# Performance work log

Hardware: AMD Instinct MI355X
Metric: run time of the kernel (lower is better)

## Reference

```python
import jax, jax.numpy as jnp
import numpy as np

B, T, IN_DIM = 128, 512, 32
H = 256            # h_dim; bidirectional -> embedding_dim D = 2*H = 512
N_EMB = 1024
BETA = 0.25


def setup_inputs() -> dict:
    key = jax.random.key(0)
    ks = jax.random.split(key, 12)
    traj = jax.random.normal(ks[0], (B, T, IN_DIM), dtype=jnp.float32)
    # variable-length padding mask: ones up to length, zeros after
    lengths = jax.random.randint(ks[1], (B,), 1, T + 1)
    mask = (jnp.arange(T)[None, :] < lengths[:, None]).astype(jnp.int32)
    s_x = 1.0 / np.sqrt(H)
    def u(k, shape):
        return jax.random.uniform(k, shape, jnp.float32, -s_x, s_x)
    # PyTorch GRU param layout: W_ih [3H, in], W_hh [3H, H], biases [3H]
    Wx_f, Wh_f = u(ks[2], (3 * H, IN_DIM)), u(ks[3], (3 * H, H))
    bx_f, bh_f = u(ks[4], (3 * H,)), u(ks[5], (3 * H,))
    Wx_b, Wh_b = u(ks[6], (3 * H, IN_DIM)), u(ks[7], (3 * H, H))
    bx_b, bh_b = u(ks[8], (3 * H,)), u(ks[9], (3 * H,))
    # codebook: nn.Embedding(n_embeddings, D) with uniform(-1/n, 1/n) init
    codebook = jax.random.uniform(ks[10], (N_EMB, 2 * H), jnp.float32,
                                  -1.0 / N_EMB, 1.0 / N_EMB)
    return {"traj": traj, "mask": mask,
            "Wx_f": Wx_f, "Wh_f": Wh_f, "bx_f": bx_f, "bh_f": bh_f,
            "Wx_b": Wx_b, "Wh_b": Wh_b, "bx_b": bx_b, "bh_b": bh_b,
            "codebook": codebook}


def _gru_dir(x, Wx, Wh, bx, bh):
    """Single-direction GRU over time (PyTorch gate math). x: [B,T,in] -> [B,T,H]."""
    b, t, _ = x.shape
    h_dim = Wh.shape[1]
    xg = jnp.einsum('bti,gi->btg', x, Wx) + bx  # precompute input gates [B,T,3H]
    def step(h, xg_t):
        hg = h @ Wh.T + bh
        xr, xz, xn = jnp.split(xg_t, 3, axis=-1)
        hr, hz, hn = jnp.split(hg, 3, axis=-1)
        r = jax.nn.sigmoid(xr + hr)
        z = jax.nn.sigmoid(xz + hz)
        n = jnp.tanh(xn + r * hn)
        h_new = (1.0 - z) * n + z * h
        return h_new, h_new
    h0 = jnp.zeros((b, h_dim), x.dtype)
    _, hs = jax.lax.scan(step, h0, jnp.swapaxes(xg, 0, 1))  # [T,B,H]
    return jnp.swapaxes(hs, 0, 1)


def _encode(traj, Wx_f, Wh_f, bx_f, bh_f, Wx_b, Wh_b, bx_b, bh_b):
    out_f = _gru_dir(traj, Wx_f, Wh_f, bx_f, bh_f)
    out_b = jnp.flip(_gru_dir(jnp.flip(traj, axis=1), Wx_b, Wh_b, bx_b, bh_b), axis=1)
    return jnp.concatenate([out_f, out_b], axis=-1)  # [B,T,2H]


def _vq(z_e, codebook, beta):
    # d(z, e) = |z|^2 + |e|^2 - 2 z.e  -> argmin over codebook
    d = (jnp.sum(z_e ** 2, axis=1, keepdims=True)
         + jnp.sum(codebook ** 2, axis=1)[None, :]
         - 2.0 * z_e @ codebook.T)                      # [B, N_EMB]
    idx = jnp.argmin(d, axis=1)                         # [B]
    z_q = codebook[idx]                                 # gather [B, D]
    loss = (jnp.mean((jax.lax.stop_gradient(z_q) - z_e) ** 2)
            + beta * jnp.mean((z_q - jax.lax.stop_gradient(z_e)) ** 2))
    z_q_st = z_e + jax.lax.stop_gradient(z_q - z_e)     # straight-through
    counts = jnp.zeros((codebook.shape[0],), z_e.dtype).at[idx].add(1.0)
    p = counts / z_e.shape[0]
    perplexity = jnp.exp(-jnp.sum(p * jnp.log(p + 1e-10)))
    return loss, z_q_st, perplexity, idx


def reference(traj, mask, Wx_f, Wh_f, bx_f, bh_f, Wx_b, Wh_b, bx_b, bh_b, codebook):
    z_e = _encode(traj, Wx_f, Wh_f, bx_f, bh_f, Wx_b, Wh_b, bx_b, bh_b)  # [B,T,2H]
    t = mask.shape[1]
    # last index where mask == 1:  T-1 - argmax(flip(mask))
    last_real_index = t - 1 - jnp.argmax(jnp.flip(mask, axis=1), axis=1)
    z_e_last = z_e[jnp.arange(z_e.shape[0]), last_real_index]            # [B,2H]
    loss, z_q, perplexity, _ = _vq(z_e_last, codebook, BETA)
    return z_q, loss, perplexity
```

## Files before the change

### kernel.cpp

```cpp
#include <hip/hip_runtime.h>
#include <math.h>

constexpr int B  = 128;
constexpr int T  = 512;
constexpr int IN = 32;
constexpr int H  = 256;
constexpr int D  = 2 * H;
constexpr int NC = 1024;

constexpr int NG   = 64;
constexpr int GW   = 4;
constexpr int SEQ  = 4;
constexpr int NTHR = 768;


__global__ void k_zero(int* __restrict__ counts, double* __restrict__ lsum) {
    const int i = blockIdx.x * 256 + threadIdx.x;
    if (i < NC) counts[i] = 0;
    if (i == 0) *lsum = 0.0;
}

__global__ void k_lengths(const int* __restrict__ mask, int* __restrict__ last) {
    const int b = blockIdx.x;
    const int t = threadIdx.x;
    int s = 0;
    #pragma unroll
    for (int m = 0; m < T / 64; ++m) s += mask[b * T + m * 64 + t];
    #pragma unroll
    for (int off = 32; off > 0; off >>= 1) s += __shfl_down(s, off, 64);
    if (t == 0) last[b] = s - 1;
}

__global__ void k_plan(const int* __restrict__ last, int* __restrict__ plan,
                       int* __restrict__ slen, int* __restrict__ glen) {
    __shared__ int ll[B];
    const int t = threadIdx.x;
    ll[t] = last[t];
    __syncthreads();
    const int lf = ll[t] + 1;
    const int lb = T - ll[t];
    int rf = 0, rb = 0;
    for (int j = 0; j < B; ++j) {
        const int ljf = ll[j] + 1, ljb = T - ll[j];
        rf += (ljf > lf) || (ljf == lf && j < t);
        rb += (ljb > lb) || (ljb == lb && j < t);
    }
    plan[rf] = t;       slen[rf] = lf;
    plan[128 + rb] = t; slen[128 + rb] = lb;
    if ((rf & 3) == 0) glen[rf >> 2] = lf;
    if ((rb & 3) == 0) glen[32 + (rb >> 2)] = lb;
}

__global__ void k_transpose(float* __restrict__ dst, const float* __restrict__ src,
                            int rows, int cols) {
    const int idx = blockIdx.x * 256 + threadIdx.x;
    const int r = idx % rows;
    const int c = idx / rows;
    dst[idx] = src[r * cols + c];
}

__global__ void k_cbn2(const float* __restrict__ cb, double* __restrict__ cbn2) {
    const int c = blockIdx.x * 256 + threadIdx.x;
    double s = 0.0;
    for (int k = 0; k < D; ++k) {
        const double e = (double)cb[c * D + k];
        s += e * e;
    }
    cbn2[c] = s;
}


__device__ __forceinline__ float sigmoidf_(float x) {
    return 1.0f / (1.0f + expf(-x));
}

__global__ __launch_bounds__(NTHR, 3) void k_gru(
    const float* __restrict__ traj,
    const float* __restrict__ Whf, const float* __restrict__ Whb,
    const float* __restrict__ Wxf, const float* __restrict__ Wxb,
    const float* __restrict__ bxf, const float* __restrict__ bhf,
    const float* __restrict__ bxb, const float* __restrict__ bhb,
    const int* __restrict__ plan, const int* __restrict__ slen,
    const int* __restrict__ glen,
    unsigned long long* __restrict__ hgt,
    float* __restrict__ ze)
{
    const int g   = blockIdx.x & 63;
    const int w   = blockIdx.x >> 6;
    const int dir = (g >= 32) ? 1 : 0;

    const float* __restrict__ Wh = dir ? Whb : Whf;
    const float* __restrict__ Wx = dir ? Wxb : Wxf;
    const float* __restrict__ bx = dir ? bxb : bxf;
    const float* __restrict__ bh = dir ? bhb : bhf;

    const int tid = threadIdx.x;
    const int kq  = tid / 96;
    const int rp  = tid - kq * 96;
    const int lr0 = 2 * rp;
    const int gi  = lr0 >> 6;
    const int Rg0 = gi * H + w * 64 + (lr0 & 63);

    __shared__ float4 h4[SEQ][64];
    __shared__ float  P [8][SEQ][194];
    __shared__ float  Px[8][SEQ][194];
    __shared__ float4 xb4[2][SEQ][8];
    __shared__ int    bbS[SEQ], lsS[SEQ];

    if (tid < SEQ) { bbS[tid] = plan[g * 4 + tid]; lsS[tid] = slen[g * 4 + tid]; }
    {
        float2* hp = (float2*)h4;
        if (tid < 512) hp[tid] = make_float2(0.0f, 0.0f);
    }
    const int L = glen[g];

    float4 wh[16];
    {
        const float4* p0 = (const float4*)(Wh + (size_t)Rg0 * 256 + kq * 32);
        const float4* p1 = (const float4*)(Wh + (size_t)(Rg0 + 1) * 256 + kq * 32);
        #pragma unroll
        for (int i = 0; i < 8; ++i) { wh[i] = p0[i]; wh[8 + i] = p1[i]; }
    }
    const float4 wx0 = *(const float4*)(Wx + Rg0 * 32 + kq * 4);
    const float4 wx1 = *(const float4*)(Wx + (Rg0 + 1) * 32 + kq * 4);

    float bxr = 0, bxz = 0, bxn = 0, bhr = 0, bhz = 0, bhn = 0;
    if (tid < 256) {
        const int j2 = tid & 63;
        bxr = bx[w * 64 + j2]; bxz = bx[H + w * 64 + j2]; bxn = bx[2 * H + w * 64 + j2];
        bhr = bh[w * 64 + j2]; bhz = bh[H + w * 64 + j2]; bhn = bh[2 * H + w * 64 + j2];
    }
    __syncthreads();
    if (tid < 128) {
        const int s = tid >> 5, i = tid & 31;
        const int t0 = dir ? (T - 1) : 0;
        ((float*)xb4)[128 + s * 32 + i] = traj[(bbS[s] * T + t0) * IN + i];
    }
    __syncthreads();

    const int u = tid - 256;

    for (int step = 1; step <= L; ++step) {
        const int buf = step & 1;
        unsigned long long* __restrict__ slab =
            hgt + (buf * NG + g) * (GW * SEQ * 64);

        float4 a0 = {0,0,0,0}, a1 = {0,0,0,0}, a2 = {0,0,0,0}, a3 = {0,0,0,0};
        float4 c0 = {0,0,0,0}, c1 = {0,0,0,0}, c2 = {0,0,0,0}, c3 = {0,0,0,0};
        #pragma unroll
        for (int i = 0; i < 8; ++i) {
            const float4 w0 = wh[i];
            const float4 w1 = wh[8 + i];
            float4 hv;
            hv = h4[0][kq * 8 + i];
            a0.x = fmaf(w0.x, hv.x, a0.x); a0.y = fmaf(w0.y, hv.y, a0.y);
            a0.z = fmaf(w0.z, hv.z, a0.z); a0.w = fmaf(w0.w, hv.w, a0.w);
            c0.x = fmaf(w1.x, hv.x, c0.x); c0.y = fmaf(w1.y, hv.y, c0.y);
            c0.z = fmaf(w1.z, hv.z, c0.z); c0.w = fmaf(w1.w, hv.w, c0.w);
            hv = h4[1][kq * 8 + i];
            a1.x = fmaf(w0.x, hv.x, a1.x); a1.y = fmaf(w0.y, hv.y, a1.y);
            a1.z = fmaf(w0.z, hv.z, a1.z); a1.w = fmaf(w0.w, hv.w, a1.w);
            c1.x = fmaf(w1.x, hv.x, c1.x); c1.y = fmaf(w1.y, hv.y, c1.y);
            c1.z = fmaf(w1.z, hv.z, c1.z); c1.w = fmaf(w1.w, hv.w, c1.w);
            hv = h4[2][kq * 8 + i];
            a2.x = fmaf(w0.x, hv.x, a2.x); a2.y = fmaf(w0.y, hv.y, a2.y);
            a2.z = fmaf(w0.z, hv.z, a2.z); a2.w = fmaf(w0.w, hv.w, a2.w);
            c2.x = fmaf(w1.x, hv.x, c2.x); c2.y = fmaf(w1.y, hv.y, c2.y);
            c2.z = fmaf(w1.z, hv.z, c2.z); c2.w = fmaf(w1.w, hv.w, c2.w);
            hv = h4[3][kq * 8 + i];
            a3.x = fmaf(w0.x, hv.x, a3.x); a3.y = fmaf(w0.y, hv.y, a3.y);
            a3.z = fmaf(w0.z, hv.z, a3.z); a3.w = fmaf(w0.w, hv.w, a3.w);
            c3.x = fmaf(w1.x, hv.x, c3.x); c3.y = fmaf(w1.y, hv.y, c3.y);
            c3.z = fmaf(w1.z, hv.z, c3.z); c3.w = fmaf(w1.w, hv.w, c3.w);
        }
        {
            float4 xv;
            float2 pv;
            xv = xb4[buf][0][kq];
            pv.x = a0.x + a0.y + a0.z + a0.w;
            pv.y = c0.x + c0.y + c0.z + c0.w;
            *(float2*)&P[kq][0][lr0] = pv;
            pv.x = wx0.x * xv.x + wx0.y * xv.y + wx0.z * xv.z + wx0.w * xv.w;
            pv.y = wx1.x * xv.x + wx1.y * xv.y + wx1.z * xv.z + wx1.w * xv.w;
            *(float2*)&Px[kq][0][lr0] = pv;
            xv = xb4[buf][1][kq];
            pv.x = a1.x + a1.y + a1.z + a1.w;
            pv.y = c1.x + c1.y + c1.z + c1.w;
            *(float2*)&P[kq][1][lr0] = pv;
            pv.x = wx0.x * xv.x + wx0.y * xv.y + wx0.z * xv.z + wx0.w * xv.w;
            pv.y = wx1.x * xv.x + wx1.y * xv.y + wx1.z * xv.z + wx1.w * xv.w;
            *(float2*)&Px[kq][1][lr0] = pv;
            xv = xb4[buf][2][kq];
            pv.x = a2.x + a2.y + a2.z + a2.w;
            pv.y = c2.x + c2.y + c2.z + c2.w;
            *(float2*)&P[kq][2][lr0] = pv;
            pv.x = wx0.x * xv.x + wx0.y * xv.y + wx0.z * xv.z + wx0.w * xv.w;
            pv.y = wx1.x * xv.x + wx1.y * xv.y + wx1.z * xv.z + wx1.w * xv.w;
            *(float2*)&Px[kq][2][lr0] = pv;
            xv = xb4[buf][3][kq];
            pv.x = a3.x + a3.y + a3.z + a3.w;
            pv.y = c3.x + c3.y + c3.z + c3.w;
            *(float2*)&P[kq][3][lr0] = pv;
            pv.x = wx0.x * xv.x + wx0.y * xv.y + wx0.z * xv.z + wx0.w * xv.w;
            pv.y = wx1.x * xv.x + wx1.y * xv.y + wx1.z * xv.z + wx1.w * xv.w;
            *(float2*)&Px[kq][3][lr0] = pv;
        }
        __syncthreads();

        if (tid < 256) {
            const int j2 = tid & 63, s = tid >> 6;
            float hr = 0.f, hz = 0.f, hn_ = 0.f, xr = 0.f, xz = 0.f, xn = 0.f;
            #pragma unroll
            for (int kk = 0; kk < 8; ++kk) {
                hr  += P [kk][s][j2];
                hz  += P [kk][s][64 + j2];
                hn_ += P [kk][s][128 + j2];
                xr  += Px[kk][s][j2];
                xz  += Px[kk][s][64 + j2];
                xn  += Px[kk][s][128 + j2];
            }
            const float r = sigmoidf_(xr + bxr + hr + bhr);
            const float z = sigmoidf_(xz + bxz + hz + bhz);
            const float n = tanhf(xn + bxn + r * (hn_ + bhn));
            const int jg = w * 64 + j2;
            const float hp = ((const float*)h4)[s * 256 + jg];
            const float hnew = (1.0f - z) * n + z * hp;
            ((float*)h4)[s * 256 + jg] = hnew;
            union { float f; unsigned ui; } cv; cv.f = hnew;
            const unsigned long long pk =
                ((unsigned long long)(unsigned)step << 32) | cv.ui;
            __hip_atomic_store(&slab[w * 256 + s * 64 + j2], pk,
                               __ATOMIC_RELAXED, __HIP_MEMORY_SCOPE_AGENT);
            if (step == lsS[s]) ze[bbS[s] * D + dir * H + jg] = hnew;
        } else {
            float xval = 0.0f;
            int xs = 0, xi = 0;
            const bool do_x = (u < 128) && (step < L);
            if (do_x) {
                xs = u >> 5; xi = u & 31;
                const int tn = dir ? (T - 1 - step) : step;
                xval = traj[(bbS[xs] * T + tn) * IN + xi];
            }
            const int p0 = u >> 8;
            const int r2 = u & 255;
            const int s0 = r2 >> 6, j0 = r2 & 63;
            const int pw0 = p0 + (p0 >= w ? 1 : 0);
            unsigned long long* ad0 = &slab[pw0 * 256 + s0 * 64 + j0];
            if (u < 256) {
                const int pw1 = 2 + (2 >= w ? 1 : 0);
                unsigned long long* ad1 = &slab[pw1 * 256 + s0 * 64 + j0];
                unsigned long long v0 = 0, v1 = 0;
                bool d0 = false, d1 = false;
                do {
                    if (!d0) { v0 = __hip_atomic_load(ad0, __ATOMIC_RELAXED,
                                   __HIP_MEMORY_SCOPE_AGENT); d0 = ((int)(v0 >> 32) >= step); }
                    if (!d1) { v1 = __hip_atomic_load(ad1, __ATOMIC_RELAXED,
                                   __HIP_MEMORY_SCOPE_AGENT); d1 = ((int)(v1 >> 32) >= step); }
                } while (!(d0 && d1));
                union { unsigned ui; float f; } e0, e1;
                e0.ui = (unsigned)v0; e1.ui = (unsigned)v1;
                ((float*)h4)[s0 * 256 + pw0 * 64 + j0] = e0.f;
                ((float*)h4)[s0 * 256 + pw1 * 64 + j0] = e1.f;
            } else {
                unsigned long long v0;
                do {
                    v0 = __hip_atomic_load(ad0, __ATOMIC_RELAXED,
                                           __HIP_MEMORY_SCOPE_AGENT);
                } while ((int)(v0 >> 32) < step);
                union { unsigned ui; float f; } e0; e0.ui = (unsigned)v0;
                ((float*)h4)[s0 * 256 + pw0 * 64 + j0] = e0.f;
            }
            if (do_x)
                ((float*)xb4)[(buf ^ 1) * 128 + xs * 32 + xi] = xval;
        }
        __syncthreads();
    }
}


__global__ __launch_bounds__(256) void k_vq(
    const float* __restrict__ ze, const float* __restrict__ cbT,
    const float* __restrict__ cb, const double* __restrict__ cbn2,
    int* __restrict__ counts, double* __restrict__ lsum,
    float* __restrict__ out)
{
    __shared__ float lz[D];
    __shared__ double ds[256];
    __shared__ int cs[256];

    const int b = blockIdx.x;
    const int t = threadIdx.x;

    lz[t]       = ze[b * D + t];
    lz[t + 256] = ze[b * D + 256 + t];
    __syncthreads();

    double best = 1e300;
    int bc = 0;
    for (int m = 0; m < NC / 256; ++m) {
        const int c = m * 256 + t;
        double s2 = 0.0;
        #pragma unroll 4
        for (int k = 0; k < D; ++k)
            s2 += (double)lz[k] * (double)cbT[k * NC + c];
        const double dist = cbn2[c] - 2.0 * s2;
        if (dist < best) { best = dist; bc = c; }
    }
    ds[t] = best; cs[t] = bc;
    __syncthreads();
    for (int s = 128; s > 0; s >>= 1) {
        if (t < s) {
            if (ds[t + s] < ds[t] || (ds[t + s] == ds[t] && cs[t + s] < cs[t])) {
                ds[t] = ds[t + s]; cs[t] = cs[t + s];
            }
        }
        __syncthreads();
    }
    const int idx = cs[0];
    __syncthreads();

    if (t == 0) atomicAdd(&counts[idx], 1);

    double loc = 0.0;
    for (int jj = t; jj < D; jj += 256) {
        const float zev = lz[jj];
        const float zqv = cb[idx * D + jj];
        out[b * D + jj] = zev + (zqv - zev);
        const double df = (double)zqv - (double)zev;
        loc += df * df;
    }
    ds[t] = loc;
    __syncthreads();
    for (int s = 128; s > 0; s >>= 1) {
        if (t < s) ds[t] += ds[t + s];
        __syncthreads();
    }
    if (t == 0) atomicAdd(lsum, ds[0]);
}

__global__ void k_final(const int* __restrict__ counts,
                        const double* __restrict__ lsum,
                        float* __restrict__ out)
{
    __shared__ double ds[256];
    const int t = threadIdx.x;
    double s = 0.0;
    for (int c = t; c < NC; c += 256) {
        const double p = (double)counts[c] / (double)B;
        s += p * log(p + 1e-10);
    }
    ds[t] = s;
    __syncthreads();
    for (int r = 128; r > 0; r >>= 1) {
        if (t < r) ds[t] += ds[t + r];
        __syncthreads();
    }
    if (t == 0) {
        out[B * D]     = (float)(lsum[0] * 1.25 / (double)(B * D));
        out[B * D + 1] = (float)exp(-ds[0]);
    }
}


extern "C" void kernel_launch(void* const* d_in, const int* in_sizes, int n_in,
                              void* d_out, int out_size, void* d_ws, size_t ws_size,
                              hipStream_t stream) {
    const float* traj = (const float*)d_in[0];
    const int*   mask = (const int*)d_in[1];
    const float* Wxf  = (const float*)d_in[2];
    const float* Whf  = (const float*)d_in[3];
    const float* bxf  = (const float*)d_in[4];
    const float* bhf  = (const float*)d_in[5];
    const float* Wxb  = (const float*)d_in[6];
    const float* Whb  = (const float*)d_in[7];
    const float* bxb  = (const float*)d_in[8];
    const float* bhb  = (const float*)d_in[9];
    const float* cb   = (const float*)d_in[10];
    float* out = (float*)d_out;

    float* ws    = (float*)d_ws;
    float* cbT   = ws;
    float* zebuf = cbT + 524288;
    unsigned long long* hgt =
        (unsigned long long*)(zebuf + 65536);
    int*   last  = (int*)(hgt + 131072);
    int*   plan  = last + 128;
    int*   slen  = plan + 256;
    int*   glen  = slen + 256;
    int*   cnts  = glen + 64;
    double* cbn2 = (double*)(cnts + 1024 + 4);
    double* lsum = cbn2 + 1024;

    k_zero<<<dim3(4), dim3(256), 0, stream>>>(cnts, lsum);
    k_lengths<<<dim3(B), dim3(64), 0, stream>>>(mask, last);
    k_plan<<<dim3(1), dim3(B), 0, stream>>>(last, plan, slen, glen);

    k_transpose<<<dim3(2048), dim3(256), 0, stream>>>(cbT, cb, NC, D);
    k_cbn2<<<dim3(4), dim3(256), 0, stream>>>(cb, cbn2);

    k_gru<<<dim3(NG * GW), dim3(NTHR), 26880, stream>>>(
        traj, Whf, Whb, Wxf, Wxb, bxf, bhf, bxb, bhb,
        plan, slen, glen, hgt, zebuf);

    k_vq<<<dim3(B), dim3(256), 0, stream>>>(zebuf, cbT, cb, cbn2, cnts, lsum, out);
    k_final<<<dim3(1), dim3(256), 0, stream>>>(cnts, lsum, out);
}
```

Baseline: 1.720 ms.

## Shrink GRU block to 512 threads with three rows per thread

Cuts the GRU block from 768 to 512 threads. Each thread now computes three recurrent weight rows instead of two, keeping 24 float4 weight registers. The next-step input load moves into the gate-update threads. The polling threads each wait on three peer slabs instead of one or two. This reduces thread count and barrier cost per step, but raises register pressure, replaces vectorised float2 shared stores with scalar ones, and makes each polling thread spin on more flags.

After: 1.857 ms. 1.08x slower.

```diff
diff --git a/kernel.cpp b/kernel.cpp
--- a/kernel.cpp
+++ b/kernel.cpp
@@ -11,7 +11,7 @@
 constexpr int NG   = 64;
 constexpr int GW   = 4;
 constexpr int SEQ  = 4;
-constexpr int NTHR = 768;
+constexpr int NTHR = 512;
 
 
 __global__ void k_zero(int* __restrict__ counts, double* __restrict__ lsum) {
@@ -74,7 +74,7 @@
     return 1.0f / (1.0f + expf(-x));
 }
 
-__global__ __launch_bounds__(NTHR, 3) void k_gru(
+__global__ __launch_bounds__(NTHR, 2) void k_gru(
     const float* __restrict__ traj,
     const float* __restrict__ Whf, const float* __restrict__ Whb,
     const float* __restrict__ Wxf, const float* __restrict__ Wxb,
@@ -95,11 +95,12 @@
     const float* __restrict__ bh = dir ? bhb : bhf;
 
     const int tid = threadIdx.x;
-    const int kq  = tid / 96;
-    const int rp  = tid - kq * 96;
-    const int lr0 = 2 * rp;
-    const int gi  = lr0 >> 6;
-    const int Rg0 = gi * H + w * 64 + (lr0 & 63);
+    const int kq  = tid >> 6;
+    const int rt  = tid & 63;
+    const int lrA = 3 * rt, lrB = lrA + 1, lrC = lrA + 2;
+    const int RA = (lrA >> 6) * H + w * 64 + (lrA & 63);
+    const int RB = (lrB >> 6) * H + w * 64 + (lrB & 63);
+    const int RC = (lrC >> 6) * H + w * 64 + (lrC & 63);
 
     __shared__ float4 h4[SEQ][64];
     __shared__ float  P [8][SEQ][194];
@@ -110,19 +111,21 @@
     if (tid < SEQ) { bbS[tid] = plan[g * 4 + tid]; lsS[tid] = slen[g * 4 + tid]; }
     {
         float2* hp = (float2*)h4;
-        if (tid < 512) hp[tid] = make_float2(0.0f, 0.0f);
+        hp[tid] = make_float2(0.0f, 0.0f);
     }
     const int L = glen[g];
 
-    float4 wh[16];
+    float4 wh[24];
     {
-        const float4* p0 = (const float4*)(Wh + (size_t)Rg0 * 256 + kq * 32);
-        const float4* p1 = (const float4*)(Wh + (size_t)(Rg0 + 1) * 256 + kq * 32);
+        const float4* pA = (const float4*)(Wh + (size_t)RA * 256 + kq * 32);
+        const float4* pB = (const float4*)(Wh + (size_t)RB * 256 + kq * 32);
+        const float4* pC = (const float4*)(Wh + (size_t)RC * 256 + kq * 32);
         #pragma unroll
-        for (int i = 0; i < 8; ++i) { wh[i] = p0[i]; wh[8 + i] = p1[i]; }
-    }
-    const float4 wx0 = *(const float4*)(Wx + Rg0 * 32 + kq * 4);
-    const float4 wx1 = *(const float4*)(Wx + (Rg0 + 1) * 32 + kq * 4);
+        for (int i = 0; i < 8; ++i) { wh[i] = pA[i]; wh[8 + i] = pB[i]; wh[16 + i] = pC[i]; }
+    }
+    const float4 wx0 = *(const float4*)(Wx + RA * 32 + kq * 4);
+    const float4 wx1 = *(const float4*)(Wx + RB * 32 + kq * 4);
+    const float4 wx2 = *(const float4*)(Wx + RC * 32 + kq * 4);
 
     float bxr = 0, bxz = 0, bxn = 0, bhr = 0, bhz = 0, bhn = 0;
     if (tid < 256) {
@@ -147,63 +150,72 @@
 
         float4 a0 = {0,0,0,0}, a1 = {0,0,0,0}, a2 = {0,0,0,0}, a3 = {0,0,0,0};
         float4 c0 = {0,0,0,0}, c1 = {0,0,0,0}, c2 = {0,0,0,0}, c3 = {0,0,0,0};
+        float4 e0 = {0,0,0,0}, e1 = {0,0,0,0}, e2 = {0,0,0,0}, e3 = {0,0,0,0};
         #pragma unroll
         for (int i = 0; i < 8; ++i) {
             const float4 w0 = wh[i];
             const float4 w1 = wh[8 + i];
+            const float4 w2 = wh[16 + i];
             float4 hv;
             hv = h4[0][kq * 8 + i];
             a0.x = fmaf(w0.x, hv.x, a0.x); a0.y = fmaf(w0.y, hv.y, a0.y);
             a0.z = fmaf(w0.z, hv.z, a0.z); a0.w = fmaf(w0.w, hv.w, a0.w);
             c0.x = fmaf(w1.x, hv.x, c0.x); c0.y = fmaf(w1.y, hv.y, c0.y);
             c0.z = fmaf(w1.z, hv.z, c0.z); c0.w = fmaf(w1.w, hv.w, c0.w);
+            e0.x = fmaf(w2.x, hv.x, e0.x); e0.y = fmaf(w2.y, hv.y, e0.y);
+            e0.z = fmaf(w2.z, hv.z, e0.z); e0.w = fmaf(w2.w, hv.w, e0.w);
             hv = h4[1][kq * 8 + i];
             a1.x = fmaf(w0.x, hv.x, a1.x); a1.y = fmaf(w0.y, hv.y, a1.y);
             a1.z = fmaf(w0.z, hv.z, a1.z); a1.w = fmaf(w0.w, hv.w, a1.w);
             c1.x = fmaf(w1.x, hv.x, c1.x); c1.y = fmaf(w1.y, hv.y, c1.y);
             c1.z = fmaf(w1.z, hv.z, c1.z); c1.w = fmaf(w1.w, hv.w, c1.w);
+            e1.x = fmaf(w2.x, hv.x, e1.x); e1.y = fmaf(w2.y, hv.y, e1.y);
+            e1.z = fmaf(w2.z, hv.z, e1.z); e1.w = fmaf(w2.w, hv.w, e1.w);
             hv = h4[2][kq * 8 + i];
             a2.x = fmaf(w0.x, hv.x, a2.x); a2.y = fmaf(w0.y, hv.y, a2.y);
             a2.z = fmaf(w0.z, hv.z, a2.z); a2.w = fmaf(w0.w, hv.w, a2.w);
             c2.x = fmaf(w1.x, hv.x, c2.x); c2.y = fmaf(w1.y, hv.y, c2.y);
             c2.z = fmaf(w1.z, hv.z, c2.z); c2.w = fmaf(w1.w, hv.w, c2.w);
+            e2.x = fmaf(w2.x, hv.x, e2.x); e2.y = fmaf(w2.y, hv.y, e2.y);
+            e2.z = fmaf(w2.z, hv.z, e2.z); e2.w = fmaf(w2.w, hv.w, e2.w);
             hv = h4[3][kq * 8 + i];
             a3.x = fmaf(w0.x, hv.x, a3.x); a3.y = fmaf(w0.y, hv.y, a3.y);
             a3.z = fmaf(w0.z, hv.z, a3.z); a3.w = fmaf(w0.w, hv.w, a3.w);
             c3.x = fmaf(w1.x, hv.x, c3.x); c3.y = fmaf(w1.y, hv.y, c3.y);
             c3.z = fmaf(w1.z, hv.z, c3.z); c3.w = fmaf(w1.w, hv.w, c3.w);
+            e3.x = fmaf(w2.x, hv.x, e3.x); e3.y = fmaf(w2.y, hv.y, e3.y);
+            e3.z = fmaf(w2.z, hv.z, e3.z); e3.w = fmaf(w2.w, hv.w, e3.w);
         }
         {
             float4 xv;
-            float2 pv;
             xv = xb4[buf][0][kq];
-            pv.x = a0.x + a0.y + a0.z + a0.w;
-            pv.y = c0.x + c0.y + c0.z + c0.w;
-            *(float2*)&P[kq][0][lr0] = pv;
-            pv.x = wx0.x * xv.x + wx0.y * xv.y + wx0.z * xv.z + wx0.w * xv.w;
-            pv.y = wx1.x * xv.x + wx1.y * xv.y + wx1.z * xv.z + wx1.w * xv.w;
-            *(float2*)&Px[kq][0][lr0] = pv;
+            P[kq][0][lrA] = a0.x + a0.y + a0.z + a0.w;
+            P[kq][0][lrB] = c0.x + c0.y + c0.z + c0.w;
+            P[kq][0][lrC] = e0.x + e0.y + e0.z + e0.w;
+            Px[kq][0][lrA] = wx0.x * xv.x + wx0.y * xv.y + wx0.z * xv.z + wx0.w * xv.w;
+            Px[kq][0][lrB] = wx1.x * xv.x + wx1.y * xv.y + wx1.z * xv.z + wx1.w * xv.w;
+            Px[kq][0][lrC] = wx2.x * xv.x + wx2.y * xv.y + wx2.z * xv.z + wx2.w * xv.w;
             xv = xb4[buf][1][kq];
-            pv.x = a1.x + a1.y + a1.z + a1.w;
-            pv.y = c1.x + c1.y + c1.z + c1.w;
-            *(float2*)&P[kq][1][lr0] = pv;
-            pv.x = wx0.x * xv.x + wx0.y * xv.y + wx0.z * xv.z + wx0.w * xv.w;
-            pv.y = wx1.x * xv.x + wx1.y * xv.y + wx1.z * xv.z + wx1.w * xv.w;
-            *(float2*)&Px[kq][1][lr0] = pv;
+            P[kq][1][lrA] = a1.x + a1.y + a1.z + a1.w;
+            P[kq][1][lrB] = c1.x + c1.y + c1.z + c1.w;
+            P[kq][1][lrC] = e1.x + e1.y + e1.z + e1.w;
+            Px[kq][1][lrA] = wx0.x * xv.x + wx0.y * xv.y + wx0.z * xv.z + wx0.w * xv.w;
+            Px[kq][1][lrB] = wx1.x * xv.x + wx1.y * xv.y + wx1.z * xv.z + wx1.w * xv.w;
+            Px[kq][1][lrC] = wx2.x * xv.x + wx2.y * xv.y + wx2.z * xv.z + wx2.w * xv.w;
             xv = xb4[buf][2][kq];
-            pv.x = a2.x + a2.y + a2.z + a2.w;
-            pv.y = c2.x + c2.y + c2.z + c2.w;
-            *(float2*)&P[kq][2][lr0] = pv;
-            pv.x = wx0.x * xv.x + wx0.y * xv.y + wx0.z * xv.z + wx0.w * xv.w;
-            pv.y = wx1.x * xv.x + wx1.y * xv.y + wx1.z * xv.z + wx1.w * xv.w;
-            *(float2*)&Px[kq][2][lr0] = pv;
+            P[kq][2][lrA] = a2.x + a2.y + a2.z + a2.w;
+            P[kq][2][lrB] = c2.x + c2.y + c2.z + c2.w;
+            P[kq][2][lrC] = e2.x + e2.y + e2.z + e2.w;
+            Px[kq][2][lrA] = wx0.x * xv.x + wx0.y * xv.y + wx0.z * xv.z + wx0.w * xv.w;
+            Px[kq][2][lrB] = wx1.x * xv.x + wx1.y * xv.y + wx1.z * xv.z + wx1.w * xv.w;
+            Px[kq][2][lrC] = wx2.x * xv.x + wx2.y * xv.y + wx2.z * xv.z + wx2.w * xv.w;
             xv = xb4[buf][3][kq];
-            pv.x = a3.x + a3.y + a3.z + a3.w;
-            pv.y = c3.x + c3.y + c3.z + c3.w;
-            *(float2*)&P[kq][3][lr0] = pv;
-            pv.x = wx0.x * xv.x + wx0.y * xv.y + wx0.z * xv.z + wx0.w * xv.w;
-            pv.y = wx1.x * xv.x + wx1.y * xv.y + wx1.z * xv.z + wx1.w * xv.w;
-            *(float2*)&Px[kq][3][lr0] = pv;
+            P[kq][3][lrA] = a3.x + a3.y + a3.z + a3.w;
+            P[kq][3][lrB] = c3.x + c3.y + c3.z + c3.w;
+            P[kq][3][lrC] = e3.x + e3.y + e3.z + e3.w;
+            Px[kq][3][lrA] = wx0.x * xv.x + wx0.y * xv.y + wx0.z * xv.z + wx0.w * xv.w;
+            Px[kq][3][lrB] = wx1.x * xv.x + wx1.y * xv.y + wx1.z * xv.z + wx1.w * xv.w;
+            Px[kq][3][lrC] = wx2.x * xv.x + wx2.y * xv.y + wx2.z * xv.z + wx2.w * xv.w;
         }
         __syncthreads();
 
@@ -232,46 +244,32 @@
             __hip_atomic_store(&slab[w * 256 + s * 64 + j2], pk,
                                __ATOMIC_RELAXED, __HIP_MEMORY_SCOPE_AGENT);
             if (step == lsS[s]) ze[bbS[s] * D + dir * H + jg] = hnew;
+            if (j2 < 32 && step < L) {
+                const int tn = dir ? (T - 1 - step) : step;
+                const float xval = traj[(bbS[s] * T + tn) * IN + j2];
+                ((float*)xb4)[(buf ^ 1) * 128 + s * 32 + j2] = xval;
+            }
         } else {
-            float xval = 0.0f;
-            int xs = 0, xi = 0;
-            const bool do_x = (u < 128) && (step < L);
-            if (do_x) {
-                xs = u >> 5; xi = u & 31;
-                const int tn = dir ? (T - 1 - step) : step;
-                xval = traj[(bbS[xs] * T + tn) * IN + xi];
-            }
-            const int p0 = u >> 8;
-            const int r2 = u & 255;
-            const int s0 = r2 >> 6, j0 = r2 & 63;
-            const int pw0 = p0 + (p0 >= w ? 1 : 0);
+            const int s0 = u >> 6, j0 = u & 63;
+            const int pw0 = (w + 1) & 3, pw1 = (w + 2) & 3, pw2 = (w + 3) & 3;
             unsigned long long* ad0 = &slab[pw0 * 256 + s0 * 64 + j0];
-            if (u < 256) {
-                const int pw1 = 2 + (2 >= w ? 1 : 0);
-                unsigned long long* ad1 = &slab[pw1 * 256 + s0 * 64 + j0];
-                unsigned long long v0 = 0, v1 = 0;
-                bool d0 = false, d1 = false;
-                do {
-                    if (!d0) { v0 = __hip_atomic_load(ad0, __ATOMIC_RELAXED,
-                                   __HIP_MEMORY_SCOPE_AGENT); d0 = ((int)(v0 >> 32) >= step); }
-                    if (!d1) { v1 = __hip_atomic_load(ad1, __ATOMIC_RELAXED,
-                                   __HIP_MEMORY_SCOPE_AGENT); d1 = ((int)(v1 >> 32) >= step); }
-                } while (!(d0 && d1));
-                union { unsigned ui; float f; } e0, e1;
-                e0.ui = (unsigned)v0; e1.ui = (unsigned)v1;
-                ((float*)h4)[s0 * 256 + pw0 * 64 + j0] = e0.f;
-                ((float*)h4)[s0 * 256 + pw1 * 64 + j0] = e1.f;
-            } else {
-                unsigned long long v0;
-                do {
-                    v0 = __hip_atomic_load(ad0, __ATOMIC_RELAXED,
-                                           __HIP_MEMORY_SCOPE_AGENT);
-                } while ((int)(v0 >> 32) < step);
-                union { unsigned ui; float f; } e0; e0.ui = (unsigned)v0;
-                ((float*)h4)[s0 * 256 + pw0 * 64 + j0] = e0.f;
-            }
-            if (do_x)
-                ((float*)xb4)[(buf ^ 1) * 128 + xs * 32 + xi] = xval;
+            unsigned long long* ad1 = &slab[pw1 * 256 + s0 * 64 + j0];
+            unsigned long long* ad2 = &slab[pw2 * 256 + s0 * 64 + j0];
+            unsigned long long v0 = 0, v1 = 0, v2 = 0;
+            bool d0 = false, d1 = false, d2 = false;
+            do {
+                if (!d0) { v0 = __hip_atomic_load(ad0, __ATOMIC_RELAXED,
+                               __HIP_MEMORY_SCOPE_AGENT); d0 = ((int)(v0 >> 32) >= step); }
+                if (!d1) { v1 = __hip_atomic_load(ad1, __ATOMIC_RELAXED,
+                               __HIP_MEMORY_SCOPE_AGENT); d1 = ((int)(v1 >> 32) >= step); }
+                if (!d2) { v2 = __hip_atomic_load(ad2, __ATOMIC_RELAXED,
+                               __HIP_MEMORY_SCOPE_AGENT); d2 = ((int)(v2 >> 32) >= step); }
+            } while (!(d0 && d1 && d2));
+            union { unsigned ui; float f; } f0, f1, f2;
+            f0.ui = (unsigned)v0; f1.ui = (unsigned)v1; f2.ui = (unsigned)v2;
+            ((float*)h4)[s0 * 256 + pw0 * 64 + j0] = f0.f;
+            ((float*)h4)[s0 * 256 + pw1 * 64 + j0] = f1.f;
+            ((float*)h4)[s0 * 256 + pw2 * 64 + j0] = f2.f;
         }
         __syncthreads();
     }
```
